# Kernel tuning notes

Measured on AMD Instinct MI355X. Metric: run time of the kernel, lower is better.

The kernel has to match this reference:

```python
import jax, jax.numpy as jnp
import numpy as np
from jax import lax

NUM_ITER = 10  # num_iterations
NUM_CLASSES = 21


def _avg_pool(x, k):
    # PyTorch F.avg_pool2d with stride=1, padding=k//2, count_include_pad=True:
    # zero-pad, sum over kxk window, divide by k*k.
    p = k // 2
    s = lax.reduce_window(x, 0.0, lax.add, (1, 1, k, k), (1, 1, 1, 1),
                          [(0, 0), (0, 0), (p, p), (p, p)])
    return s / float(k * k)


def _edge_weight(image):
    # grayscale -> sobel gradients -> exp(-|grad|)
    gray = 0.299 * image[:, 0:1] + 0.587 * image[:, 1:2] + 0.114 * image[:, 2:3]
    sx = jnp.array([[-1, 0, 1], [-2, 0, 2], [-1, 0, 1]], dtype=image.dtype).reshape(1, 1, 3, 3)
    sy = jnp.array([[-1, -2, -1], [0, 0, 0], [1, 2, 1]], dtype=image.dtype).reshape(1, 1, 3, 3)
    dn = ('NCHW', 'OIHW', 'NCHW')
    gx = lax.conv_general_dilated(gray, sx, (1, 1), [(1, 1), (1, 1)], dimension_numbers=dn)
    gy = lax.conv_general_dilated(gray, sy, (1, 1), [(1, 1), (1, 1)], dimension_numbers=dn)
    mag = jnp.sqrt(gx ** 2 + gy ** 2 + 1e-6)
    return jnp.exp(-mag)  # [B,1,H,W]


def setup_inputs() -> dict:
    key = jax.random.key(0)
    k1, k2 = jax.random.split(key)
    B, C, H, W = 8, NUM_CLASSES, 512, 512
    unary = jax.random.normal(k1, (B, C, H, W), dtype=jnp.float32)
    image = jax.random.uniform(k2, (B, 3, H, W), dtype=jnp.float32)
    compatibility = jnp.eye(C, dtype=jnp.float32)
    spatial_weight = jnp.asarray(3.0, dtype=jnp.float32)
    bilateral_weight = jnp.asarray(5.0, dtype=jnp.float32)
    return {"unary": unary, "image": image, "compatibility": compatibility,
            "spatial_weight": spatial_weight, "bilateral_weight": bilateral_weight}


def reference(unary, image, compatibility, spatial_weight, bilateral_weight):
    # edge weights depend only on the image -> compute once (identical math each iter)
    edge = _edge_weight(image)                  # [B,1,H,W]
    norm = _avg_pool(edge, 3) + 1e-6            # bilateral normalizer
    sw = jnp.maximum(spatial_weight, 0.0)
    bw = jnp.maximum(bilateral_weight, 0.0)

    Q = jax.nn.softmax(unary, axis=1)
    for _ in range(NUM_ITER):
        Q_spatial = _avg_pool(Q, 5)
        Q_bilateral = _avg_pool(Q * edge, 3) / norm
        messages = sw * Q_spatial + bw * Q_bilateral
        # bmm(compat [C,C], messages [B,C,HW]) == einsum over class dim
        compat = jnp.einsum('cd,bdhw->bchw', compatibility, messages)
        Q = jax.nn.softmax(unary - compat, axis=1)
    return Q
```

## Files before the change

### kernel.cpp

```cpp
#include <hip/hip_runtime.h>
#include <hip/hip_fp16.h>

#define PLANE 262144
#define NC 21
#define NB 8
#define NPIX (NB*PLANE)

__device__ __forceinline__ float2 h2f(unsigned int u) {
  union { unsigned int u; __half2 h; } x; x.u = u;
  return __half22float2(x.h);
}
__device__ __forceinline__ unsigned int f2h(float a, float b) {
  union { unsigned int u; __half2 h; } x;
  x.h = __floats2half2_rn(a, b);
  return x.u;
}

__global__ __launch_bounds__(256)
void k_edge(const float* __restrict__ img, __half* __restrict__ edge16) {
  int id = blockIdx.x*256 + threadIdx.x;
  int b = id >> 18;
  int rem = id & (PLANE-1);
  int y = rem >> 9, x = rem & 511;
  const float* ib = img + (size_t)b*3*PLANE;
  float g[3][3];
#pragma unroll
  for (int dy=0; dy<3; ++dy)
#pragma unroll
    for (int dx=0; dx<3; ++dx) {
      int yy = y+dy-1, xx = x+dx-1;
      float v = 0.f;
      if (yy>=0 && yy<512 && xx>=0 && xx<512) {
        int o = (yy<<9)|xx;
        v = 0.299f*ib[o] + 0.587f*ib[o+PLANE] + 0.114f*ib[o+2*PLANE];
      }
      g[dy][dx]=v;
    }
  float gxv = (g[0][2]-g[0][0]) + 2.f*(g[1][2]-g[1][0]) + (g[2][2]-g[2][0]);
  float gyv = (g[2][0]-g[0][0]) + 2.f*(g[2][1]-g[0][1]) + (g[2][2]-g[0][2]);
  float mag = sqrtf(gxv*gxv + gyv*gyv + 1e-6f);
  edge16[id] = __float2half(__expf(-mag));
}

__global__ __launch_bounds__(256)
void k_rnorm(const __half* __restrict__ edge16, float* __restrict__ rnorm) {
  int id = blockIdx.x*256 + threadIdx.x;
  int b = id >> 18;
  int rem = id & (PLANE-1);
  int y = rem >> 9, x = rem & 511;
  const __half* eb = edge16 + (size_t)b*PLANE;
  float s = 0.f;
#pragma unroll
  for (int dy=-1; dy<=1; ++dy)
#pragma unroll
    for (int dx=-1; dx<=1; ++dx) {
      int yy = y+dy, xx = x+dx;
      if (yy>=0 && yy<512 && xx>=0 && xx<512) s += __half2float(eb[(yy<<9)|xx]);
    }
  rnorm[id] = 1.f/(s*(1.f/9.f) + 1e-6f);
}

__global__ void k_flag(const float* __restrict__ compat, int* __restrict__ flag) {
  __shared__ int ok;
  if (threadIdx.x==0) ok = 1;
  __syncthreads();
  int bad = 0;
  for (int i = threadIdx.x; i < NC*NC; i += 256) {
    float exp = ((i/NC) == (i%NC)) ? 1.f : 0.f;
    if (compat[i] != exp) bad = 1;
  }
  if (bad) atomicAnd(&ok, 0);
  __syncthreads();
  if (threadIdx.x==0) flag[0] = ok;
}

__global__ __launch_bounds__(256)
void k_cvt(const float* __restrict__ u, __half* __restrict__ u16) {
  size_t q = (size_t)blockIdx.x*256 + threadIdx.x;
  float4 v = reinterpret_cast<const float4*>(u)[q];
  uint2 w; w.x = f2h(v.x, v.y); w.y = f2h(v.z, v.w);
  reinterpret_cast<uint2*>(u16)[q] = w;
}

__global__ __launch_bounds__(256)
void k_softmax0(const float* __restrict__ unary, __half* __restrict__ Y) {
  int q = blockIdx.x*256 + threadIdx.x;
  int b = q >> 16;
  int rem = q & 65535;
  size_t base = (size_t)b*NC*(PLANE>>2) + rem;
  const float4* up = reinterpret_cast<const float4*>(unary);
  float v[NC][4];
  float mx0=-3e38f,mx1=-3e38f,mx2=-3e38f,mx3=-3e38f;
#pragma unroll
  for (int c=0;c<NC;++c) {
    float4 t = up[base + (size_t)c*(PLANE>>2)];
    v[c][0]=t.x; v[c][1]=t.y; v[c][2]=t.z; v[c][3]=t.w;
    mx0=fmaxf(mx0,t.x); mx1=fmaxf(mx1,t.y); mx2=fmaxf(mx2,t.z); mx3=fmaxf(mx3,t.w);
  }
  float s0=0,s1=0,s2=0,s3=0;
#pragma unroll
  for (int c=0;c<NC;++c) {
    float e0=__expf(v[c][0]-mx0), e1=__expf(v[c][1]-mx1);
    float e2=__expf(v[c][2]-mx2), e3=__expf(v[c][3]-mx3);
    v[c][0]=e0; v[c][1]=e1; v[c][2]=e2; v[c][3]=e3;
    s0+=e0; s1+=e1; s2+=e2; s3+=e3;
  }
  float r0=1.f/s0, r1=1.f/s1, r2=1.f/s2, r3=1.f/s3;
  uint2* yp = reinterpret_cast<uint2*>(Y);
#pragma unroll
  for (int c=0;c<NC;++c) {
    uint2 w; w.x=f2h(v[c][0]*r0, v[c][1]*r1); w.y=f2h(v[c][2]*r2, v[c][3]*r3);
    yp[base + (size_t)c*(PLANE>>2)] = w;
  }
}


#define LOAD_U2(c, u0,u1) \
  float u0,u1; \
  if (U16) { unsigned int w_ = reinterpret_cast<const unsigned int*>(uptr)[hbase + (size_t)(c)*ch]; \
    float2 t_=h2f(w_); u0=t_.x; u1=t_.y; } \
  else { float2 v_ = reinterpret_cast<const float2*>(uptr)[hbase + (size_t)(c)*ch]; \
    u0=v_.x; u1=v_.y; }

#define CROW 72
#define TROWS 12
#define CTILE (TROWS*CROW)

#define COMPUTE_CH(c, buf, uu, uf) do { \
    const __half* qrow0_ = (buf) + ty*CROW + lx2; \
    __half2 a0_ = __float2half2_rn(0.f); \
    __half2 a1_ = a0_, a2_ = a0_; \
    float ce0=0.f,ce1=0.f,ce2=0.f,ce3=0.f; \
    _Pragma("unroll") \
    for (int dy=0;dy<5;++dy) { \
      const __half2* qrow = reinterpret_cast<const __half2*>(qrow0_ + dy*CROW); \
      __half2 q0=qrow[0], q1=qrow[1], q2=qrow[2]; \
      a0_ = __hadd2(a0_, q0); a1_ = __hadd2(a1_, q1); a2_ = __hadd2(a2_, q2); \
      if (dy>=1 && dy<=3) { \
        ce0 += __high2float(q0)*ew[dy-1][0]; \
        ce1 += __low2float (q1)*ew[dy-1][1]; \
        ce2 += __high2float(q1)*ew[dy-1][2]; \
        ce3 += __low2float (q2)*ew[dy-1][3]; \
      } \
    } \
    float cs0=__low2float(a0_), cs1=__high2float(a0_); \
    float cs2=__low2float(a1_), cs3=__high2float(a1_); \
    float cs4=__low2float(a2_), cs5=__high2float(a2_); \
    float v0 = cs0+cs1+cs2+cs3+cs4; \
    float v1 = v0 - cs0 + cs5; \
    float w0 = ce0+ce1+ce2; \
    float w1 = ce1+ce2+ce3; \
    float m0 = csw*v0 + cb0*w0; \
    float m1 = csw*v1 + cb1*w1; \
    float u0c,u1c; \
    if (U16) { float2 t_=h2f(uu); u0c=t_.x; u1c=t_.y; } \
    else     { u0c=(uf).x; u1c=(uf).y; } \
    float lv0, lv1; \
    if (fl) { lv0=u0c-m0; lv1=u1c-m1; mx0=fmaxf(mx0,lv0); mx1=fmaxf(mx1,lv1); } \
    else    { lv0=m0; lv1=m1; } \
    lsm[c][tid] = make_float2(lv0, lv1); \
  } while(0)

template<bool U16, bool OUTF32>
__global__ __launch_bounds__(256)
void k_iter(const __half* __restrict__ Qin,
            void* __restrict__ Qout,
            const void* __restrict__ uptr,
            const __half* __restrict__ edge16,
            const float* __restrict__ rnorm,
            const float* __restrict__ swp,
            const float* __restrict__ bwp,
            const float* __restrict__ compat,
            const int* __restrict__ flag)
{
  __shared__ __half qbuf[2][2][CTILE];
  __shared__ __half et[CTILE];
  __shared__ float2 lsm[NC][256];

  const int tid = threadIdx.x;
  const int tx = tid & 31;
  const int ty = tid >> 5;
  const int x0 = blockIdx.x << 6;
  const int y0 = blockIdx.y << 3;
  const int b  = blockIdx.z;

  const int slot = tid;
  const int sr = slot / 18;
  const int si = slot - sr*18;
  const int sy = y0 - 2 + sr;
  const int sx = x0 - 4 + (si<<2);
  const bool sact = (slot < 216);
  const bool sval = sact && (sy>=0) && (sy<512) && (sx>=0) && (sx<512);
  const int  goff = (sy<<9) + sx;
  const int  loff = sr*CROW + (si<<2);

  const int gy  = y0 + ty;
  const int gx  = x0 + (tx<<1);
  const int pix = (gy<<9) | gx;

  const float2 rn = *reinterpret_cast<const float2*>(rnorm + (size_t)b*PLANE + pix);
  const float sw  = fmaxf(swp[0], 0.f);
  const float bw  = fmaxf(bwp[0], 0.f);
  const int fl = flag[0];

  const size_t hbase = (((size_t)b*NC*PLANE) + (size_t)pix) >> 1;
  const size_t ch = PLANE >> 1;

  const __half* qb = Qin + (size_t)b*NC*PLANE;
  unsigned int uc0=0, uc1=0; float2 uf0=make_float2(0.f,0.f), uf1=uf0;
  if (U16) {
    uc0 = reinterpret_cast<const unsigned int*>(uptr)[hbase];
    uc1 = reinterpret_cast<const unsigned int*>(uptr)[hbase + ch];
  } else {
    uf0 = reinterpret_cast<const float2*>(uptr)[hbase];
    uf1 = reinterpret_cast<const float2*>(uptr)[hbase + ch];
  }
  {
    const __half* ep = edge16 + (size_t)b*PLANE;
    uint2 we = make_uint2(0u,0u), w0 = we, w1 = we;
    if (sval) {
      we = *reinterpret_cast<const uint2*>(ep + goff);
      w0 = *reinterpret_cast<const uint2*>(qb + goff);
      w1 = *reinterpret_cast<const uint2*>(qb + PLANE + goff);
    }
    if (sact) {
      *reinterpret_cast<uint2*>(et + loff) = we;
      *reinterpret_cast<uint2*>(qbuf[0][0] + loff) = w0;
      *reinterpret_cast<uint2*>(qbuf[0][1] + loff) = w1;
    }
  }
  __syncthreads();

  const float csw = sw * 0.04f;
  const float b9  = bw * (1.f/9.f);
  const float cb0 = b9*rn.x, cb1 = b9*rn.y;

  const int lx2 = (tx<<1) + 2;

  float ew[3][4];
#pragma unroll
  for (int dy=0;dy<3;++dy) {
    const unsigned int* erow = reinterpret_cast<const unsigned int*>(et + (ty+1+dy)*CROW + lx2);
    float2 e0 = h2f(erow[0]);
    float2 e1 = h2f(erow[1]);
    float2 e2 = h2f(erow[2]);
    ew[dy][0]=e0.y; ew[dy][1]=e1.x; ew[dy][2]=e1.y; ew[dy][3]=e2.x;
  }

  float mx0=-3e38f, mx1=-3e38f;

#pragma unroll
  for (int cp=0; cp<11; ++cp) {
    const int c0 = 2*cp, c1 = 2*cp+1;

    uint2 wn0 = make_uint2(0u,0u), wn1 = wn0;
    unsigned int un0=0, un1=0; float2 unf0=make_float2(0.f,0.f), unf1=unf0;
    if (c0+2 < NC) {
      if (sval) wn0 = *reinterpret_cast<const uint2*>(qb + (size_t)(c0+2)*PLANE + goff);
      if (U16) un0 = reinterpret_cast<const unsigned int*>(uptr)[hbase + (size_t)(c0+2)*ch];
      else     unf0 = reinterpret_cast<const float2*>(uptr)[hbase + (size_t)(c0+2)*ch];
    }
    if (c1+2 < NC) {
      if (sval) wn1 = *reinterpret_cast<const uint2*>(qb + (size_t)(c1+2)*PLANE + goff);
      if (U16) un1 = reinterpret_cast<const unsigned int*>(uptr)[hbase + (size_t)(c1+2)*ch];
      else     unf1 = reinterpret_cast<const float2*>(uptr)[hbase + (size_t)(c1+2)*ch];
    }

    COMPUTE_CH(c0, qbuf[cp&1][0], uc0, uf0);
    if (c1 < NC) COMPUTE_CH(c1, qbuf[cp&1][1], uc1, uf1);

    if (c0+2 < NC) {
      if (sact) {
        *reinterpret_cast<uint2*>(qbuf[(cp+1)&1][0] + loff) = wn0;
        if (c1+2 < NC) *reinterpret_cast<uint2*>(qbuf[(cp+1)&1][1] + loff) = wn1;
      }
      __syncthreads();
    }
    uc0=un0; uc1=un1; uf0=unf0; uf1=unf1;
  }

  if (fl) {
    float s0=0.f, s1=0.f;
#pragma unroll
    for (int c=0;c<NC;++c) {
      float2 lv = lsm[c][tid];
      float e0=__expf(lv.x-mx0), e1=__expf(lv.y-mx1);
      lsm[c][tid]=make_float2(e0,e1);
      s0+=e0; s1+=e1;
    }
    float r0=1.f/s0, r1=1.f/s1;
#pragma unroll
    for (int c=0;c<NC;++c) {
      float2 ev = lsm[c][tid];
      float o0=ev.x*r0, o1=ev.y*r1;
      if (OUTF32) {
        reinterpret_cast<float2*>(Qout)[hbase + (size_t)c*ch] = make_float2(o0,o1);
      } else {
        reinterpret_cast<unsigned int*>(Qout)[hbase + (size_t)c*ch] = f2h(o0,o1);
      }
    }
  } else {
    float mxa=-3e38f, mxb=-3e38f;
#pragma unroll 1
    for (int c=0;c<NC;++c) {
      float a0=0.f,a1=0.f;
#pragma unroll
      for (int d=0;d<NC;++d) { float cf=compat[c*NC+d]; float2 lv=lsm[d][tid]; a0+=cf*lv.x; a1+=cf*lv.y; }
      LOAD_U2(c, u0,u1)
      mxa=fmaxf(mxa,u0-a0); mxb=fmaxf(mxb,u1-a1);
    }
    float s0=0.f,s1=0.f;
#pragma unroll 1
    for (int c=0;c<NC;++c) {
      float a0=0.f,a1=0.f;
#pragma unroll
      for (int d=0;d<NC;++d) { float cf=compat[c*NC+d]; float2 lv=lsm[d][tid]; a0+=cf*lv.x; a1+=cf*lv.y; }
      LOAD_U2(c, u0,u1)
      s0+=__expf(u0-a0-mxa); s1+=__expf(u1-a1-mxb);
    }
    float r0=1.f/s0, r1=1.f/s1;
#pragma unroll 1
    for (int c=0;c<NC;++c) {
      float a0=0.f,a1=0.f;
#pragma unroll
      for (int d=0;d<NC;++d) { float cf=compat[c*NC+d]; float2 lv=lsm[d][tid]; a0+=cf*lv.x; a1+=cf*lv.y; }
      LOAD_U2(c, u0,u1)
      float o0=__expf(u0-a0-mxa)*r0, o1=__expf(u1-a1-mxb)*r1;
      if (OUTF32) {
        reinterpret_cast<float2*>(Qout)[hbase + (size_t)c*ch] = make_float2(o0,o1);
      } else {
        reinterpret_cast<unsigned int*>(Qout)[hbase + (size_t)c*ch] = f2h(o0,o1);
      }
    }
  }
}

extern "C" void kernel_launch(void* const* d_in, const int* in_sizes, int n_in,
                              void* d_out, int out_size, void* d_ws, size_t ws_size,
                              hipStream_t stream)
{
  const float* unary  = (const float*)d_in[0];
  const float* image  = (const float*)d_in[1];
  const float* compat = (const float*)d_in[2];
  const float* swp    = (const float*)d_in[3];
  const float* bwp    = (const float*)d_in[4];

  char* ws = (char*)d_ws;
  __half* X      = (__half*)(ws + 0);
  __half* edge16 = (__half*)(ws + 88080384);
  float*  rnorm  = (float*) (ws + 92274688);
  int*    flag   = (int*)   (ws + 100663296);
  __half* u16    = (__half*)(ws + 100663552);
  if (ws_size < (size_t)100663552) return;
  const bool use_u16 = (ws_size >= (size_t)188743936);

  __half* Y  = (__half*)d_out;
  float* out = (float*)d_out;

  k_edge   <<<dim3(8192), dim3(256), 0, stream>>>(image, edge16);
  k_rnorm  <<<dim3(8192), dim3(256), 0, stream>>>(edge16, rnorm);
  k_flag   <<<dim3(1),    dim3(256), 0, stream>>>(compat, flag);
  if (use_u16) k_cvt<<<dim3(43008), dim3(256), 0, stream>>>(unary, u16);
  k_softmax0<<<dim3(2048), dim3(256), 0, stream>>>(unary, Y);

  const void* up = use_u16 ? (const void*)u16 : (const void*)unary;
  dim3 gi(8, 64, NB), bi(256);
  for (int it = 1; it <= 10; ++it) {
    const __half* qin = (it & 1) ? Y : X;
    if (it == 10) {
      if (use_u16) k_iter<true , true ><<<gi,bi,0,stream>>>(qin,(void*)out,up,edge16,rnorm,swp,bwp,compat,flag);
      else         k_iter<false, true ><<<gi,bi,0,stream>>>(qin,(void*)out,up,edge16,rnorm,swp,bwp,compat,flag);
    } else {
      void* qout = (it & 1) ? (void*)X : (void*)Y;
      if (use_u16) k_iter<true , false><<<gi,bi,0,stream>>>(qin,qout,up,edge16,rnorm,swp,bwp,compat,flag);
      else         k_iter<false, false><<<gi,bi,0,stream>>>(qin,qout,up,edge16,rnorm,swp,bwp,compat,flag);
    }
  }
}
```

Baseline: 1.173 ms.

## Split iteration kernel into identity and general variants with online softmax

```diff
diff --git a/kernel.cpp b/kernel.cpp
--- a/kernel.cpp
+++ b/kernel.cpp
@@ -74,26 +74,25 @@
   if (threadIdx.x==0) flag[0] = ok;
 }
 
+template<bool WU16>
 __global__ __launch_bounds__(256)
-void k_cvt(const float* __restrict__ u, __half* __restrict__ u16) {
-  size_t q = (size_t)blockIdx.x*256 + threadIdx.x;
-  float4 v = reinterpret_cast<const float4*>(u)[q];
-  uint2 w; w.x = f2h(v.x, v.y); w.y = f2h(v.z, v.w);
-  reinterpret_cast<uint2*>(u16)[q] = w;
-}
-
-__global__ __launch_bounds__(256)
-void k_softmax0(const float* __restrict__ unary, __half* __restrict__ Y) {
+void k_prep0(const float* __restrict__ unary, __half* __restrict__ Y,
+             __half* __restrict__ u16) {
   int q = blockIdx.x*256 + threadIdx.x;
   int b = q >> 16;
   int rem = q & 65535;
   size_t base = (size_t)b*NC*(PLANE>>2) + rem;
   const float4* up = reinterpret_cast<const float4*>(unary);
+  uint2* u16p = reinterpret_cast<uint2*>(u16);
   float v[NC][4];
   float mx0=-3e38f,mx1=-3e38f,mx2=-3e38f,mx3=-3e38f;
 #pragma unroll
   for (int c=0;c<NC;++c) {
     float4 t = up[base + (size_t)c*(PLANE>>2)];
+    if (WU16) {
+      uint2 w; w.x=f2h(t.x,t.y); w.y=f2h(t.z,t.w);
+      u16p[base + (size_t)c*(PLANE>>2)] = w;
+    }
     v[c][0]=t.x; v[c][1]=t.y; v[c][2]=t.z; v[c][3]=t.w;
     mx0=fmaxf(mx0,t.x); mx1=fmaxf(mx1,t.y); mx2=fmaxf(mx2,t.z); mx3=fmaxf(mx3,t.w);
   }
@@ -111,6 +110,193 @@
   for (int c=0;c<NC;++c) {
     uint2 w; w.x=f2h(v[c][0]*r0, v[c][1]*r1); w.y=f2h(v[c][2]*r2, v[c][3]*r3);
     yp[base + (size_t)c*(PLANE>>2)] = w;
+  }
+}
+
+#define CROW 72
+#define TROWS 12
+#define CTILE (TROWS*CROW)
+
+
+#define COMPUTE_CHF(c, buf, uu, uf) do { \
+    const __half* qrow0_ = (buf) + ty*CROW + lx2; \
+    __half2 a0_ = __float2half2_rn(0.f); \
+    __half2 a1_ = a0_, a2_ = a0_; \
+    float ce0=0.f,ce1=0.f,ce2=0.f,ce3=0.f; \
+    _Pragma("unroll") \
+    for (int dy=0;dy<5;++dy) { \
+      const __half2* qrow = reinterpret_cast<const __half2*>(qrow0_ + dy*CROW); \
+      __half2 q0=qrow[0], q1=qrow[1], q2=qrow[2]; \
+      a0_ = __hadd2(a0_, q0); a1_ = __hadd2(a1_, q1); a2_ = __hadd2(a2_, q2); \
+      if (dy>=1 && dy<=3) { \
+        ce0 += __high2float(q0)*ew[dy-1][0]; \
+        ce1 += __low2float (q1)*ew[dy-1][1]; \
+        ce2 += __high2float(q1)*ew[dy-1][2]; \
+        ce3 += __low2float (q2)*ew[dy-1][3]; \
+      } \
+    } \
+    float cs0=__low2float(a0_), cs1=__high2float(a0_); \
+    float cs2=__low2float(a1_), cs3=__high2float(a1_); \
+    float cs4=__low2float(a2_), cs5=__high2float(a2_); \
+    float v0 = cs0+cs1+cs2+cs3+cs4; \
+    float v1 = v0 - cs0 + cs5; \
+    float w0 = ce0+ce1+ce2; \
+    float w1 = ce1+ce2+ce3; \
+    float mg0 = csw*v0 + cb0*w0; \
+    float mg1 = csw*v1 + cb1*w1; \
+    float u0c,u1c; \
+    if (U16) { float2 t_=h2f(uu); u0c=t_.x; u1c=t_.y; } \
+    else     { u0c=(uf).x; u1c=(uf).y; } \
+    float l0_ = u0c - mg0, l1_ = u1c - mg1; \
+    float d0_ = l0_ - rmx0, d1_ = l1_ - rmx1; \
+    if (d0_ > 8.f || d1_ > 8.f) { \
+      float sc0_ = (d0_ > 8.f) ? __expf(-d0_) : 1.f; \
+      float sc1_ = (d1_ > 8.f) ? __expf(-d1_) : 1.f; \
+      _Pragma("unroll 1") \
+      for (int dd=0; dd<(c); ++dd) { \
+        float2 pv_ = h2f(psm[dd][tid]); \
+        psm[dd][tid] = f2h(pv_.x*sc0_, pv_.y*sc1_); \
+      } \
+      sr0 *= sc0_; sr1 *= sc1_; \
+      if (d0_ > 8.f) { rmx0 = l0_; d0_ = 0.f; } \
+      if (d1_ > 8.f) { rmx1 = l1_; d1_ = 0.f; } \
+    } \
+    float p0_ = __expf(d0_), p1_ = __expf(d1_); \
+    sr0 += p0_; sr1 += p1_; \
+    psm[(c)][tid] = f2h(p0_, p1_); \
+  } while(0)
+
+template<bool U16, bool OUTF32>
+__global__ __launch_bounds__(256)
+void k_iter_f(const __half* __restrict__ Qin,
+              void* __restrict__ Qout,
+              const void* __restrict__ uptr,
+              const __half* __restrict__ edge16,
+              const float* __restrict__ rnorm,
+              const float* __restrict__ swp,
+              const float* __restrict__ bwp,
+              const float* __restrict__ compat,
+              const int* __restrict__ flag)
+{
+  __shared__ __half qbuf[2][2][CTILE];
+  __shared__ __half et[CTILE];
+  __shared__ unsigned int psm[NC][256];
+
+  const int fl = flag[0];
+  if (!fl) return;
+
+  const int tid = threadIdx.x;
+  const int tx = tid & 31;
+  const int ty = tid >> 5;
+  const int x0 = blockIdx.x << 6;
+  const int y0 = blockIdx.y << 3;
+  const int b  = blockIdx.z;
+
+  const int slot = tid;
+  const int sr_ = slot / 18;
+  const int si = slot - sr_*18;
+  const int sy = y0 - 2 + sr_;
+  const int sx = x0 - 4 + (si<<2);
+  const bool sact = (slot < 216);
+  const bool sval = sact && (sy>=0) && (sy<512) && (sx>=0) && (sx<512);
+  const int  goff = (sy<<9) + sx;
+  const int  loff = sr_*CROW + (si<<2);
+
+  const int gy  = y0 + ty;
+  const int gx  = x0 + (tx<<1);
+  const int pix = (gy<<9) | gx;
+
+  const float2 rn = *reinterpret_cast<const float2*>(rnorm + (size_t)b*PLANE + pix);
+  const float sw  = fmaxf(swp[0], 0.f);
+  const float bw  = fmaxf(bwp[0], 0.f);
+
+  const size_t hbase = (((size_t)b*NC*PLANE) + (size_t)pix) >> 1;
+  const size_t ch = PLANE >> 1;
+
+  const __half* qb = Qin + (size_t)b*NC*PLANE;
+  unsigned int uc0=0, uc1=0; float2 uf0=make_float2(0.f,0.f), uf1=uf0;
+  if (U16) {
+    uc0 = reinterpret_cast<const unsigned int*>(uptr)[hbase];
+    uc1 = reinterpret_cast<const unsigned int*>(uptr)[hbase + ch];
+  } else {
+    uf0 = reinterpret_cast<const float2*>(uptr)[hbase];
+    uf1 = reinterpret_cast<const float2*>(uptr)[hbase + ch];
+  }
+  {
+    const __half* ep = edge16 + (size_t)b*PLANE;
+    uint2 we = make_uint2(0u,0u), w0 = we, w1 = we;
+    if (sval) {
+      we = *reinterpret_cast<const uint2*>(ep + goff);
+      w0 = *reinterpret_cast<const uint2*>(qb + goff);
+      w1 = *reinterpret_cast<const uint2*>(qb + PLANE + goff);
+    }
+    if (sact) {
+      *reinterpret_cast<uint2*>(et + loff) = we;
+      *reinterpret_cast<uint2*>(qbuf[0][0] + loff) = w0;
+      *reinterpret_cast<uint2*>(qbuf[0][1] + loff) = w1;
+    }
+  }
+  __syncthreads();
+
+  const float csw = sw * 0.04f;
+  const float b9  = bw * (1.f/9.f);
+  const float cb0 = b9*rn.x, cb1 = b9*rn.y;
+
+  const int lx2 = (tx<<1) + 2;
+
+  float ew[3][4];
+#pragma unroll
+  for (int dy=0;dy<3;++dy) {
+    const unsigned int* erow = reinterpret_cast<const unsigned int*>(et + (ty+1+dy)*CROW + lx2);
+    float2 e0 = h2f(erow[0]);
+    float2 e1 = h2f(erow[1]);
+    float2 e2 = h2f(erow[2]);
+    ew[dy][0]=e0.y; ew[dy][1]=e1.x; ew[dy][2]=e1.y; ew[dy][3]=e2.x;
+  }
+
+  float rmx0=-3e38f, rmx1=-3e38f;
+  float sr0=0.f, sr1=0.f;
+
+#pragma unroll
+  for (int cp=0; cp<11; ++cp) {
+    const int c0 = 2*cp, c1 = 2*cp+1;
+
+    uint2 wn0 = make_uint2(0u,0u), wn1 = wn0;
+    unsigned int un0=0, un1=0; float2 unf0=make_float2(0.f,0.f), unf1=unf0;
+    if (c0+2 < NC) {
+      if (sval) wn0 = *reinterpret_cast<const uint2*>(qb + (size_t)(c0+2)*PLANE + goff);
+      if (U16) un0 = reinterpret_cast<const unsigned int*>(uptr)[hbase + (size_t)(c0+2)*ch];
+      else     unf0 = reinterpret_cast<const float2*>(uptr)[hbase + (size_t)(c0+2)*ch];
+    }
+    if (c1+2 < NC) {
+      if (sval) wn1 = *reinterpret_cast<const uint2*>(qb + (size_t)(c1+2)*PLANE + goff);
+      if (U16) un1 = reinterpret_cast<const unsigned int*>(uptr)[hbase + (size_t)(c1+2)*ch];
+      else     unf1 = reinterpret_cast<const float2*>(uptr)[hbase + (size_t)(c1+2)*ch];
+    }
+
+    COMPUTE_CHF(c0, qbuf[cp&1][0], uc0, uf0);
+    if (c1 < NC) COMPUTE_CHF(c1, qbuf[cp&1][1], uc1, uf1);
+
+    if (c0+2 < NC) {
+      if (sact) {
+        *reinterpret_cast<uint2*>(qbuf[(cp+1)&1][0] + loff) = wn0;
+        if (c1+2 < NC) *reinterpret_cast<uint2*>(qbuf[(cp+1)&1][1] + loff) = wn1;
+      }
+      __syncthreads();
+    }
+    uc0=un0; uc1=un1; uf0=unf0; uf1=unf1;
+  }
+
+  float r0 = 1.f/sr0, r1 = 1.f/sr1;
+#pragma unroll
+  for (int c=0;c<NC;++c) {
+    float2 pv = h2f(psm[c][tid]);
+    float o0 = pv.x*r0, o1 = pv.y*r1;
+    if (OUTF32) {
+      reinterpret_cast<float2*>(Qout)[hbase + (size_t)c*ch] = make_float2(o0,o1);
+    } else {
+      reinterpret_cast<unsigned int*>(Qout)[hbase + (size_t)c*ch] = f2h(o0,o1);
+    }
   }
 }
 
@@ -122,11 +308,7 @@
   else { float2 v_ = reinterpret_cast<const float2*>(uptr)[hbase + (size_t)(c)*ch]; \
     u0=v_.x; u1=v_.y; }
 
-#define CROW 72
-#define TROWS 12
-#define CTILE (TROWS*CROW)
-
-#define COMPUTE_CH(c, buf, uu, uf) do { \
+#define COMPUTE_CHG(c, buf, uu, uf) do { \
     const __half* qrow0_ = (buf) + ty*CROW + lx2; \
     __half2 a0_ = __float2half2_rn(0.f); \
     __half2 a1_ = a0_, a2_ = a0_; \
@@ -152,30 +334,27 @@
     float w1 = ce1+ce2+ce3; \
     float m0 = csw*v0 + cb0*w0; \
     float m1 = csw*v1 + cb1*w1; \
-    float u0c,u1c; \
-    if (U16) { float2 t_=h2f(uu); u0c=t_.x; u1c=t_.y; } \
-    else     { u0c=(uf).x; u1c=(uf).y; } \
-    float lv0, lv1; \
-    if (fl) { lv0=u0c-m0; lv1=u1c-m1; mx0=fmaxf(mx0,lv0); mx1=fmaxf(mx1,lv1); } \
-    else    { lv0=m0; lv1=m1; } \
-    lsm[c][tid] = make_float2(lv0, lv1); \
+    lsm[c][tid] = make_float2(m0, m1); \
   } while(0)
 
 template<bool U16, bool OUTF32>
 __global__ __launch_bounds__(256)
-void k_iter(const __half* __restrict__ Qin,
-            void* __restrict__ Qout,
-            const void* __restrict__ uptr,
-            const __half* __restrict__ edge16,
-            const float* __restrict__ rnorm,
-            const float* __restrict__ swp,
-            const float* __restrict__ bwp,
-            const float* __restrict__ compat,
-            const int* __restrict__ flag)
+void k_iter_gen(const __half* __restrict__ Qin,
+                void* __restrict__ Qout,
+                const void* __restrict__ uptr,
+                const __half* __restrict__ edge16,
+                const float* __restrict__ rnorm,
+                const float* __restrict__ swp,
+                const float* __restrict__ bwp,
+                const float* __restrict__ compat,
+                const int* __restrict__ flag)
 {
   __shared__ __half qbuf[2][2][CTILE];
   __shared__ __half et[CTILE];
   __shared__ float2 lsm[NC][256];
+
+  const int fl = flag[0];
+  if (fl) return;
 
   const int tid = threadIdx.x;
   const int tx = tid & 31;
@@ -185,14 +364,14 @@
   const int b  = blockIdx.z;
 
   const int slot = tid;
-  const int sr = slot / 18;
-  const int si = slot - sr*18;
-  const int sy = y0 - 2 + sr;
+  const int sr_ = slot / 18;
+  const int si = slot - sr_*18;
+  const int sy = y0 - 2 + sr_;
   const int sx = x0 - 4 + (si<<2);
   const bool sact = (slot < 216);
   const bool sval = sact && (sy>=0) && (sy<512) && (sx>=0) && (sx<512);
   const int  goff = (sy<<9) + sx;
-  const int  loff = sr*CROW + (si<<2);
+  const int  loff = sr_*CROW + (si<<2);
 
   const int gy  = y0 + ty;
   const int gx  = x0 + (tx<<1);
@@ -201,20 +380,11 @@
   const float2 rn = *reinterpret_cast<const float2*>(rnorm + (size_t)b*PLANE + pix);
   const float sw  = fmaxf(swp[0], 0.f);
   const float bw  = fmaxf(bwp[0], 0.f);
-  const int fl = flag[0];
 
   const size_t hbase = (((size_t)b*NC*PLANE) + (size_t)pix) >> 1;
   const size_t ch = PLANE >> 1;
 
   const __half* qb = Qin + (size_t)b*NC*PLANE;
-  unsigned int uc0=0, uc1=0; float2 uf0=make_float2(0.f,0.f), uf1=uf0;
-  if (U16) {
-    uc0 = reinterpret_cast<const unsigned int*>(uptr)[hbase];
-    uc1 = reinterpret_cast<const unsigned int*>(uptr)[hbase + ch];
-  } else {
-    uf0 = reinterpret_cast<const float2*>(uptr)[hbase];
-    uf1 = reinterpret_cast<const float2*>(uptr)[hbase + ch];
-  }
   {
     const __half* ep = edge16 + (size_t)b*PLANE;
     uint2 we = make_uint2(0u,0u), w0 = we, w1 = we;
@@ -247,27 +417,15 @@
     ew[dy][0]=e0.y; ew[dy][1]=e1.x; ew[dy][2]=e1.y; ew[dy][3]=e2.x;
   }
 
-  float mx0=-3e38f, mx1=-3e38f;
-
 #pragma unroll
   for (int cp=0; cp<11; ++cp) {
     const int c0 = 2*cp, c1 = 2*cp+1;
-
     uint2 wn0 = make_uint2(0u,0u), wn1 = wn0;
-    unsigned int un0=0, un1=0; float2 unf0=make_float2(0.f,0.f), unf1=unf0;
-    if (c0+2 < NC) {
-      if (sval) wn0 = *reinterpret_cast<const uint2*>(qb + (size_t)(c0+2)*PLANE + goff);
-      if (U16) un0 = reinterpret_cast<const unsigned int*>(uptr)[hbase + (size_t)(c0+2)*ch];
-      else     unf0 = reinterpret_cast<const float2*>(uptr)[hbase + (size_t)(c0+2)*ch];
-    }
-    if (c1+2 < NC) {
-      if (sval) wn1 = *reinterpret_cast<const uint2*>(qb + (size_t)(c1+2)*PLANE + goff);
-      if (U16) un1 = reinterpret_cast<const unsigned int*>(uptr)[hbase + (size_t)(c1+2)*ch];
-      else     unf1 = reinterpret_cast<const float2*>(uptr)[hbase + (size_t)(c1+2)*ch];
-    }
-
-    COMPUTE_CH(c0, qbuf[cp&1][0], uc0, uf0);
-    if (c1 < NC) COMPUTE_CH(c1, qbuf[cp&1][1], uc1, uf1);
+    if (c0+2 < NC && sval) wn0 = *reinterpret_cast<const uint2*>(qb + (size_t)(c0+2)*PLANE + goff);
+    if (c1+2 < NC && sval) wn1 = *reinterpret_cast<const uint2*>(qb + (size_t)(c1+2)*PLANE + goff);
+
+    COMPUTE_CHG(c0, qbuf[cp&1][0], 0, 0);
+    if (c1 < NC) COMPUTE_CHG(c1, qbuf[cp&1][1], 0, 0);
 
     if (c0+2 < NC) {
       if (sact) {
@@ -276,61 +434,38 @@
       }
       __syncthreads();
     }
-    uc0=un0; uc1=un1; uf0=unf0; uf1=unf1;
-  }
-
-  if (fl) {
-    float s0=0.f, s1=0.f;
-#pragma unroll
-    for (int c=0;c<NC;++c) {
-      float2 lv = lsm[c][tid];
-      float e0=__expf(lv.x-mx0), e1=__expf(lv.y-mx1);
-      lsm[c][tid]=make_float2(e0,e1);
-      s0+=e0; s1+=e1;
-    }
-    float r0=1.f/s0, r1=1.f/s1;
-#pragma unroll
-    for (int c=0;c<NC;++c) {
-      float2 ev = lsm[c][tid];
-      float o0=ev.x*r0, o1=ev.y*r1;
-      if (OUTF32) {
-        reinterpret_cast<float2*>(Qout)[hbase + (size_t)c*ch] = make_float2(o0,o1);
-      } else {
-        reinterpret_cast<unsigned int*>(Qout)[hbase + (size_t)c*ch] = f2h(o0,o1);
-      }
-    }
-  } else {
-    float mxa=-3e38f, mxb=-3e38f;
+  }
+
+  float mxa=-3e38f, mxb=-3e38f;
 #pragma unroll 1
-    for (int c=0;c<NC;++c) {
-      float a0=0.f,a1=0.f;
-#pragma unroll
-      for (int d=0;d<NC;++d) { float cf=compat[c*NC+d]; float2 lv=lsm[d][tid]; a0+=cf*lv.x; a1+=cf*lv.y; }
-      LOAD_U2(c, u0,u1)
-      mxa=fmaxf(mxa,u0-a0); mxb=fmaxf(mxb,u1-a1);
-    }
-    float s0=0.f,s1=0.f;
+  for (int c=0;c<NC;++c) {
+    float a0=0.f,a1=0.f;
+#pragma unroll
+    for (int d=0;d<NC;++d) { float cf=compat[c*NC+d]; float2 lv=lsm[d][tid]; a0+=cf*lv.x; a1+=cf*lv.y; }
+    LOAD_U2(c, u0,u1)
+    mxa=fmaxf(mxa,u0-a0); mxb=fmaxf(mxb,u1-a1);
+  }
+  float s0=0.f,s1=0.f;
 #pragma unroll 1
-    for (int c=0;c<NC;++c) {
-      float a0=0.f,a1=0.f;
-#pragma unroll
-      for (int d=0;d<NC;++d) { float cf=compat[c*NC+d]; float2 lv=lsm[d][tid]; a0+=cf*lv.x; a1+=cf*lv.y; }
-      LOAD_U2(c, u0,u1)
-      s0+=__expf(u0-a0-mxa); s1+=__expf(u1-a1-mxb);
-    }
-    float r0=1.f/s0, r1=1.f/s1;
+  for (int c=0;c<NC;++c) {
+    float a0=0.f,a1=0.f;
+#pragma unroll
+    for (int d=0;d<NC;++d) { float cf=compat[c*NC+d]; float2 lv=lsm[d][tid]; a0+=cf*lv.x; a1+=cf*lv.y; }
+    LOAD_U2(c, u0,u1)
+    s0+=__expf(u0-a0-mxa); s1+=__expf(u1-a1-mxb);
+  }
+  float r0=1.f/s0, r1=1.f/s1;
 #pragma unroll 1
-    for (int c=0;c<NC;++c) {
-      float a0=0.f,a1=0.f;
-#pragma unroll
-      for (int d=0;d<NC;++d) { float cf=compat[c*NC+d]; float2 lv=lsm[d][tid]; a0+=cf*lv.x; a1+=cf*lv.y; }
-      LOAD_U2(c, u0,u1)
-      float o0=__expf(u0-a0-mxa)*r0, o1=__expf(u1-a1-mxb)*r1;
-      if (OUTF32) {
-        reinterpret_cast<float2*>(Qout)[hbase + (size_t)c*ch] = make_float2(o0,o1);
-      } else {
-        reinterpret_cast<unsigned int*>(Qout)[hbase + (size_t)c*ch] = f2h(o0,o1);
-      }
+  for (int c=0;c<NC;++c) {
+    float a0=0.f,a1=0.f;
+#pragma unroll
+    for (int d=0;d<NC;++d) { float cf=compat[c*NC+d]; float2 lv=lsm[d][tid]; a0+=cf*lv.x; a1+=cf*lv.y; }
+    LOAD_U2(c, u0,u1)
+    float o0=__expf(u0-a0-mxa)*r0, o1=__expf(u1-a1-mxb)*r1;
+    if (OUTF32) {
+      reinterpret_cast<float2*>(Qout)[hbase + (size_t)c*ch] = make_float2(o0,o1);
+    } else {
+      reinterpret_cast<unsigned int*>(Qout)[hbase + (size_t)c*ch] = f2h(o0,o1);
     }
   }
 }
@@ -360,20 +495,30 @@
   k_edge   <<<dim3(8192), dim3(256), 0, stream>>>(image, edge16);
   k_rnorm  <<<dim3(8192), dim3(256), 0, stream>>>(edge16, rnorm);
   k_flag   <<<dim3(1),    dim3(256), 0, stream>>>(compat, flag);
-  if (use_u16) k_cvt<<<dim3(43008), dim3(256), 0, stream>>>(unary, u16);
-  k_softmax0<<<dim3(2048), dim3(256), 0, stream>>>(unary, Y);
+  if (use_u16) k_prep0<true ><<<dim3(2048), dim3(256), 0, stream>>>(unary, Y, u16);
+  else         k_prep0<false><<<dim3(2048), dim3(256), 0, stream>>>(unary, Y, u16);
 
   const void* up = use_u16 ? (const void*)u16 : (const void*)unary;
   dim3 gi(8, 64, NB), bi(256);
   for (int it = 1; it <= 10; ++it) {
     const __half* qin = (it & 1) ? Y : X;
     if (it == 10) {
-      if (use_u16) k_iter<true , true ><<<gi,bi,0,stream>>>(qin,(void*)out,up,edge16,rnorm,swp,bwp,compat,flag);
-      else         k_iter<false, true ><<<gi,bi,0,stream>>>(qin,(void*)out,up,edge16,rnorm,swp,bwp,compat,flag);
+      if (use_u16) {
+        k_iter_f  <true , true ><<<gi,bi,0,stream>>>(qin,(void*)out,up,edge16,rnorm,swp,bwp,compat,flag);
+        k_iter_gen<true , true ><<<gi,bi,0,stream>>>(qin,(void*)out,up,edge16,rnorm,swp,bwp,compat,flag);
+      } else {
+        k_iter_f  <false, true ><<<gi,bi,0,stream>>>(qin,(void*)out,up,edge16,rnorm,swp,bwp,compat,flag);
+        k_iter_gen<false, true ><<<gi,bi,0,stream>>>(qin,(void*)out,up,edge16,rnorm,swp,bwp,compat,flag);
+      }
     } else {
       void* qout = (it & 1) ? (void*)X : (void*)Y;
-      if (use_u16) k_iter<true , false><<<gi,bi,0,stream>>>(qin,qout,up,edge16,rnorm,swp,bwp,compat,flag);
-      else         k_iter<false, false><<<gi,bi,0,stream>>>(qin,qout,up,edge16,rnorm,swp,bwp,compat,flag);
-    }
-  }
-}
+      if (use_u16) {
+        k_iter_f  <true , false><<<gi,bi,0,stream>>>(qin,qout,up,edge16,rnorm,swp,bwp,compat,flag);
+        k_iter_gen<true , false><<<gi,bi,0,stream>>>(qin,qout,up,edge16,rnorm,swp,bwp,compat,flag);
+      } else {
+        k_iter_f  <false, false><<<gi,bi,0,stream>>>(qin,qout,up,edge16,rnorm,swp,bwp,compat,flag);
+        k_iter_gen<false, false><<<gi,bi,0,stream>>>(qin,qout,up,edge16,rnorm,swp,bwp,compat,flag);
+      }
+    }
+  }
+}
```

Result: faster. 1.103 ms (-6.0%).
